# Performance work log

Hardware: AMD Instinct MI355X
Metric: run time of the kernel (lower is better)

Reference implementation:

```python
import jax, jax.numpy as jnp
import numpy as np

GRID = 480  # grid extent for both x and y voxel indices


def setup_inputs() -> dict:
    key = jax.random.key(0)
    k = jax.random.split(key, 8)
    B, N, FD, H1, H2, D = 4, 100000, 3, 128, 256, 64
    scale = 0.05
    pt_fea = jax.random.normal(k[0], (B, N, FD), dtype=jnp.float32)
    xy_ind = jax.random.randint(k[1], (B, N, 2), 0, GRID, dtype=jnp.int32)
    W1 = jax.random.normal(k[2], (FD, H1), dtype=jnp.float32) * scale
    b1 = jnp.zeros((H1,), dtype=jnp.float32)
    W2 = jax.random.normal(k[3], (H1, H2), dtype=jnp.float32) * scale
    b2 = jnp.zeros((H2,), dtype=jnp.float32)
    W3 = jax.random.normal(k[4], (H2, D), dtype=jnp.float32) * scale
    b3 = jnp.zeros((D,), dtype=jnp.float32)
    return {"pt_fea": pt_fea, "xy_ind": xy_ind, "W1": W1, "b1": b1,
            "W2": W2, "b2": b2, "W3": W3, "b3": b3}


def reference(pt_fea, xy_ind, W1, b1, W2, b2, W3, b3):
    B, N, FD = pt_fea.shape
    flat = pt_fea.reshape(B * N, FD)
    # pad xy_ind with batch id -> (b, x, y) per point
    bidx = jnp.repeat(jnp.arange(B, dtype=xy_ind.dtype), N)
    xy = xy_ind.reshape(B * N, 2)
    # lexicographic linear encoding so sorted linear order == torch.unique(dim=0) row order
    lin = (bidx.astype(jnp.int32) * GRID + xy[:, 0]) * GRID + xy[:, 1]
    unq_lin, unq_inv = jnp.unique(lin, return_inverse=True)
    M = int(unq_lin.shape[0])  # concrete: indices are concrete (eager unique)
    unq = jnp.stack([unq_lin // (GRID * GRID),
                     (unq_lin // GRID) % GRID,
                     unq_lin % GRID], axis=1)
    # per-point MLP: 3 -> 128 -> 256 -> 64
    h = jax.nn.relu(flat @ W1 + b1)
    h = jax.nn.relu(h @ W2 + b2)
    feat = h @ W3 + b3
    # scatter_max pooling per unique voxel
    pooled = jax.ops.segment_max(feat, unq_inv.reshape(-1), num_segments=M)
    return unq, pooled
```

## Files before the change

kernel.cpp:

```cpp
#include <hip/hip_runtime.h>
#include <hip/hip_bf16.h>

#define GRIDW 480
#define CELLS_PER_B (GRIDW*GRIDW)
#define NCELL (4*CELLS_PER_B)
#define NPTS  400000
#define NPB   100000
#define H1D 128
#define H2D 256
#define DD 64
#define SCAN_BLK 900
#define NTILE 6250
#define GRIDP 512
#define NSUB  25000
#define CNT_NB 1563

typedef unsigned short u16;
typedef __attribute__((ext_vector_type(8))) short bf16x8;
typedef __attribute__((ext_vector_type(4))) float f32x4;
typedef __attribute__((ext_vector_type(4))) unsigned u32x4;
typedef __attribute__((ext_vector_type(2))) unsigned u32x2;

static __device__ __forceinline__ u16 f2bf(float f){
  unsigned u = __float_as_uint(f);
  unsigned r = u + 0x7FFFu + ((u>>16)&1u);
  return (u16)(r>>16);
}
static __device__ __forceinline__ float bf2f(u16 b){
  return __uint_as_float(((unsigned)b) << 16);
}
static __device__ __forceinline__ unsigned cvt_pk_bf16(float lo, float hi){
  unsigned r;
  asm("v_cvt_pk_bf16_f32 %0, %1, %2" : "=v"(r) : "v"(lo), "v"(hi));
  return r;
}

static __device__ __forceinline__ void pack_one(int e, const float* W2, const float* W3,
                                                u16* bp2, u16* bp3){
  if (e < 32768){
    int j = e & 7, c = (e>>3)&15, ko = (e>>7)&15, n = e>>11;
    bp2[e] = f2bf(W2[(ko*8+j)*H2D + n*16 + c]);
  } else {
    int e3 = e - 32768;
    int j = e3 & 7, c = (e3>>3)&15, ko = (e3>>7)&31, n = e3>>12;
    bp3[e3] = f2bf(W3[(ko*8+j)*DD + n*16 + c]);
  }
}

__global__ void k_countpack(const int* __restrict__ xy, unsigned* __restrict__ counts,
                            const float* __restrict__ W2, const float* __restrict__ W3,
                            u16* __restrict__ bp2, u16* __restrict__ bp3){
  int b = blockIdx.x;
  if (b < CNT_NB){
    int p = b*256 + threadIdx.x;
    if (p < NPTS){
      int bb = p / NPB;
      int x = xy[2*p], y = xy[2*p+1];
      atomicAdd(&counts[(bb*GRIDW + x)*GRIDW + y], 1u);
    }
  } else {
    int e = (b - CNT_NB)*256 + threadIdx.x;
    if (e < 49152) pack_one(e, W2, W3, bp2, bp3);
  }
}

__global__ void k_scan2(const unsigned* __restrict__ counts,
                        unsigned* __restrict__ rankF, unsigned* __restrict__ rankC,
                        unsigned* __restrict__ bsumF, unsigned* __restrict__ bsumC){
  __shared__ unsigned shF[256], shC[256];
  int tid = threadIdx.x;
  int base = blockIdx.x*1024 + tid*4;
  unsigned c0=counts[base], c1=counts[base+1], c2=counts[base+2], c3=counts[base+3];
  unsigned f0=c0?1u:0u, f1=c1?1u:0u, f2=c2?1u:0u, f3=c3?1u:0u;
  unsigned sF=f0+f1+f2+f3, sC=c0+c1+c2+c3;
  shF[tid]=sF; shC[tid]=sC; __syncthreads();
  for (int off=1; off<256; off<<=1){
    unsigned tF = (tid>=off) ? shF[tid-off] : 0u;
    unsigned tC = (tid>=off) ? shC[tid-off] : 0u;
    __syncthreads();
    shF[tid] += tF; shC[tid] += tC;
    __syncthreads();
  }
  unsigned eF = shF[tid]-sF, eC = shC[tid]-sC;
  if (tid==255){ bsumF[blockIdx.x]=shF[255]; bsumC[blockIdx.x]=shC[255]; }
  rankF[base]=eF; rankF[base+1]=eF+f0; rankF[base+2]=eF+f0+f1; rankF[base+3]=eF+f0+f1+f2;
  rankC[base]=eC; rankC[base+1]=eC+c0; rankC[base+2]=eC+c0+c1; rankC[base+3]=eC+c0+c1+c2;
}

__global__ void k_scan_bsum2(unsigned* __restrict__ bsumF, unsigned* __restrict__ bsumC){
  __shared__ unsigned shF[1024], shC[1024];
  int tid = threadIdx.x;
  unsigned vF = (tid<SCAN_BLK) ? bsumF[tid] : 0u;
  unsigned vC = (tid<SCAN_BLK) ? bsumC[tid] : 0u;
  shF[tid]=vF; shC[tid]=vC; __syncthreads();
  for (int off=1; off<1024; off<<=1){
    unsigned tF = (tid>=off) ? shF[tid-off] : 0u;
    unsigned tC = (tid>=off) ? shC[tid-off] : 0u;
    __syncthreads();
    shF[tid] += tF; shC[tid] += tC;
    __syncthreads();
  }
  if (tid<SCAN_BLK){ bsumF[tid]=shF[tid]-vF; bsumC[tid]=shC[tid]-vC; }
}

__global__ void k_emit2(const unsigned* __restrict__ counts,
                        unsigned* __restrict__ rankF, unsigned* __restrict__ rankC,
                        const unsigned* __restrict__ bsumF, const unsigned* __restrict__ bsumC,
                        float* __restrict__ out){
  int i = blockIdx.x*256 + threadIdx.x;
  if (i >= NCELL) return;
  unsigned rF = rankF[i] + bsumF[i>>10];
  unsigned rC = rankC[i] + bsumC[i>>10];
  rankF[i] = rF; rankC[i] = rC;
  unsigned c = counts[i];
  if (c){
    int b = i / CELLS_PER_B;
    int rem = i - b*CELLS_PER_B;
    int x = rem / GRIDW;
    int y = rem - x*GRIDW;
    float* o = out + 3u*rF;
    o[0]=(float)b; o[1]=(float)x; o[2]=(float)y;
  }
}

__global__ void k_scatterp(const int* __restrict__ xy, unsigned* __restrict__ cursor,
                           const unsigned* __restrict__ rankF,
                           unsigned* __restrict__ perm, unsigned* __restrict__ vox){
  int p = blockIdx.x*256 + threadIdx.x;
  if (p >= NPTS) return;
  int b = p / NPB;
  int x = xy[2*p], y = xy[2*p+1];
  int cell = (b*GRIDW+x)*GRIDW + y;
  unsigned slot = atomicAdd(&cursor[cell], 1u);
  perm[slot] = (unsigned)p;
  vox[slot]  = rankF[cell];
}

__global__ __launch_bounds__(256,2) void k_mlpp(
    const float* __restrict__ pt, const unsigned* __restrict__ perm,
    const unsigned* __restrict__ vox,
    const u16* __restrict__ bp2, const u16* __restrict__ bp3,
    const float* __restrict__ W1, const float* __restrict__ b1,
    const float* __restrict__ b2, const float* __restrict__ b3,
    float* __restrict__ outp,
    unsigned* __restrict__ pvf, unsigned* __restrict__ pvl,
    u16* __restrict__ pmf, u16* __restrict__ pml)
{
  __shared__ __attribute__((aligned(16))) u16 h1s[64*128];
  __shared__ __attribute__((aligned(16))) u16 h2s[2][64*64];
  __shared__ __attribute__((aligned(16))) u16 w3s[16384];
  __shared__ __attribute__((aligned(16))) float cf[832];
  __shared__ __attribute__((aligned(16))) float in_s[192];
  __shared__ unsigned vox_s[64];

  const int tid  = threadIdx.x;
  const int lane = tid & 63;
  const int w    = tid >> 6;
  const int g    = lane >> 4;
  const int p    = lane & 15;
  const int wn   = w & 1;
  const int wp   = w >> 1;
  const int oct  = tid & 15;

  for (int i = tid; i < 2048; i += 256)
    *(u32x4*)((char*)w3s + i*16) = *(const u32x4*)((const char*)bp3 + i*16);
  for (int i = tid; i < 832; i += 256){
    float v;
    if (i < 384) v = W1[i];
    else if (i < 512) v = b1[i-384];
    else if (i < 768) v = b2[i-512];
    else v = b3[i-768];
    cf[i] = v;
  }

  bf16x8 wf2[32];
  #pragma unroll
  for (int c=0;c<4;++c)
    #pragma unroll
    for (int nn=0;nn<2;++nn)
      #pragma unroll
      for (int t=0;t<4;++t){
        int ngl = c*4 + 2*wn + nn;
        wf2[(c*2+nn)*4+t] = *(const bf16x8*)(bp2 + (((ngl*16 + t*4 + g)*16) + p)*8);
      }

  int tile = blockIdx.x;
  unsigned pmN = 0;
  float pf0=0.f, pf1=0.f, pf2=0.f;
  if (tid < 64){
    unsigned pm0 = perm[(size_t)tile*64 + tid];
    const float* q = pt + 3*(size_t)pm0;
    pf0 = q[0]; pf1 = q[1]; pf2 = q[2];
    if (tile + GRIDP < NTILE) pmN = perm[(size_t)(tile+GRIDP)*64 + tid];
  }
  __syncthreads();

  for (; tile < NTILE; tile += GRIDP){
    if (tid < 64){ in_s[tid*3]=pf0; in_s[tid*3+1]=pf1; in_s[tid*3+2]=pf2; }
    unsigned vr = 0;
    if (tid < 64) vr = vox[(size_t)tile*64 + tid];
    __syncthreads();
    if (tid < 64 && tile + GRIDP < NTILE){
      const float* q = pt + 3*(size_t)pmN;
      pf0 = q[0]; pf1 = q[1]; pf2 = q[2];
    }
    unsigned pmN2 = 0;
    if (tid < 64 && tile + 2*GRIDP < NTILE)
      pmN2 = perm[(size_t)(tile+2*GRIDP)*64 + tid];

    {
      f32x4 w1v[3][2], b1v[2];
      #pragma unroll
      for (int f=0;f<3;++f){
        w1v[f][0] = *(const f32x4*)&cf[f*128 + oct*8];
        w1v[f][1] = *(const f32x4*)&cf[f*128 + oct*8 + 4];
      }
      b1v[0] = *(const f32x4*)&cf[384 + oct*8];
      b1v[1] = *(const f32x4*)&cf[384 + oct*8 + 4];
      #pragma unroll
      for (int q=0;q<4;++q){
        int row = q*16 + (tid>>4);
        float x0 = in_s[row*3+0], x1 = in_s[row*3+1], x2 = in_s[row*3+2];
        f32x4 a0 = b1v[0], a1 = b1v[1];
        #pragma unroll
        for (int i=0;i<4;++i){
          a0[i] = fmaf(x0, w1v[0][0][i], a0[i]);
          a1[i] = fmaf(x0, w1v[0][1][i], a1[i]);
          a0[i] = fmaf(x1, w1v[1][0][i], a0[i]);
          a1[i] = fmaf(x1, w1v[1][1][i], a1[i]);
          a0[i] = fmaf(x2, w1v[2][0][i], a0[i]);
          a1[i] = fmaf(x2, w1v[2][1][i], a1[i]);
          a0[i] = fmaxf(a0[i], 0.f);
          a1[i] = fmaxf(a1[i], 0.f);
        }
        u32x4 ov;
        ov[0] = cvt_pk_bf16(a0[0], a0[1]);
        ov[1] = cvt_pk_bf16(a0[2], a0[3]);
        ov[2] = cvt_pk_bf16(a1[0], a1[1]);
        ov[3] = cvt_pk_bf16(a1[2], a1[3]);
        unsigned byte = ((unsigned)row<<8) + (unsigned)oct*16u;
        byte ^= (unsigned)(row&7) << 4;
        *(u32x4*)((char*)h1s + byte) = ov;
      }
    }
    if (tid < 64) vox_s[tid] = vr;
    __syncthreads();

    bf16x8 hf[2][4];
    #pragma unroll
    for (int pp=0;pp<2;++pp){
      int row = (2*wp+pp)*16 + p;
      #pragma unroll
      for (int t=0;t<4;++t){
        unsigned byte = ((unsigned)row<<8) + (unsigned)t*64u + (unsigned)g*16u;
        byte ^= (unsigned)(row&7) << 4;
        hf[pp][t] = *(const bf16x8*)((const char*)h1s + byte);
      }
    }

    f32x4 acc3[2][2];
    #pragma unroll
    for (int a=0;a<2;++a)
      #pragma unroll
      for (int b=0;b<2;++b){ acc3[a][b][0]=0.f; acc3[a][b][1]=0.f; acc3[a][b][2]=0.f; acc3[a][b][3]=0.f; }

    #pragma unroll
    for (int c=0;c<4;++c){
      f32x4 acc2[2][2];
      #pragma unroll
      for (int a=0;a<2;++a)
        #pragma unroll
        for (int b=0;b<2;++b){ acc2[a][b][0]=0.f; acc2[a][b][1]=0.f; acc2[a][b][2]=0.f; acc2[a][b][3]=0.f; }
      #pragma unroll
      for (int t=0;t<4;++t)
        #pragma unroll
        for (int nn=0;nn<2;++nn)
          #pragma unroll
          for (int pp=0;pp<2;++pp)
            acc2[nn][pp] = __builtin_amdgcn_mfma_f32_16x16x32_bf16(
                wf2[(c*2+nn)*4+t], hf[pp][t], acc2[nn][pp], 0, 0, 0);
      u16* h2 = h2s[c & 1];
      #pragma unroll
      for (int nn=0;nn<2;++nn){
        f32x4 b2v = *(const f32x4*)&cf[512 + c*64 + (2*wn+nn)*16 + g*4];
        #pragma unroll
        for (int pp=0;pp<2;++pp){
          int point = (2*wp+pp)*16 + p;
          float e0 = fmaxf(acc2[nn][pp][0] + b2v[0], 0.f);
          float e1 = fmaxf(acc2[nn][pp][1] + b2v[1], 0.f);
          float e2 = fmaxf(acc2[nn][pp][2] + b2v[2], 0.f);
          float e3 = fmaxf(acc2[nn][pp][3] + b2v[3], 0.f);
          u32x2 o2; o2[0] = cvt_pk_bf16(e0, e1); o2[1] = cvt_pk_bf16(e2, e3);
          unsigned byte = (unsigned)point*128u + (unsigned)((2*wn+nn)*32 + g*8);
          byte ^= (unsigned)(point&7) << 4;
          *(u32x2*)((char*)h2 + byte) = o2;
        }
      }
      __syncthreads();
      #pragma unroll
      for (int t2=0;t2<2;++t2){
        bf16x8 w3f[2], h2f[2];
        #pragma unroll
        for (int dn=0;dn<2;++dn){
          int dt = 2*wn + dn;
          unsigned wb = (unsigned)(((dt*32 + (c*2+t2)*4 + g)*16 + p)*16);
          w3f[dn] = *(const bf16x8*)((const char*)w3s + wb);
        }
        #pragma unroll
        for (int pp=0;pp<2;++pp){
          int point = (2*wp+pp)*16 + p;
          unsigned byte = (unsigned)point*128u + (unsigned)t2*64u + (unsigned)g*16u;
          byte ^= (unsigned)(point&7) << 4;
          h2f[pp] = *(const bf16x8*)((const char*)h2 + byte);
        }
        #pragma unroll
        for (int dn=0;dn<2;++dn)
          #pragma unroll
          for (int pp=0;pp<2;++pp)
            acc3[dn][pp] = __builtin_amdgcn_mfma_f32_16x16x32_bf16(
                w3f[dn], h2f[pp], acc3[dn][pp], 0, 0, 0);
      }
    }

    #pragma unroll
    for (int dn=0;dn<2;++dn){
      f32x4 b3v = *(const f32x4*)&cf[768 + (2*wn+dn)*16 + g*4];
      #pragma unroll
      for (int pp=0;pp<2;++pp){
        int point = (2*wp+pp)*16 + p;
        float e0 = acc3[dn][pp][0] + b3v[0];
        float e1 = acc3[dn][pp][1] + b3v[1];
        float e2 = acc3[dn][pp][2] + b3v[2];
        float e3 = acc3[dn][pp][3] + b3v[3];
        u32x2 o2; o2[0] = cvt_pk_bf16(e0, e1); o2[1] = cvt_pk_bf16(e2, e3);
        unsigned byte = (unsigned)point*128u + (unsigned)((2*wn+dn)*32 + g*8);
        byte ^= (unsigned)(point&7) << 4;
        *(u32x2*)((char*)h2s[0] + byte) = o2;
      }
    }
    __syncthreads();

    {
      int st = tile*4 + w;
      float val[16]; unsigned vid[16];
      #pragma unroll
      for (int r=0;r<16;++r){
        int row = w*16 + r;
        unsigned byte = (unsigned)row*128u + (unsigned)lane*2u;
        byte ^= (unsigned)(row&7) << 4;
        val[r] = bf2f(*(const u16*)((const char*)h2s[0] + byte));
        vid[r] = vox_s[row];
      }
      float m = val[0];
      unsigned vprev = vid[0];
      int runstart = 0;
      #pragma unroll
      for (int r=1;r<16;++r){
        if (vid[r] != vprev){
          if (runstart == 0){
            pmf[(size_t)st*64 + lane] = (u16)(__float_as_uint(m)>>16);
            if (lane==0) pvf[st] = vprev;
          } else {
            outp[(size_t)vprev*64 + lane] = m;
          }
          m = val[r]; runstart = r; vprev = vid[r];
        } else m = fmaxf(m, val[r]);
      }
      pml[(size_t)st*64 + lane] = (u16)(__float_as_uint(m)>>16);
      if (lane==0) pvl[st] = vprev;
      if (runstart == 0){
        pmf[(size_t)st*64 + lane] = (u16)(__float_as_uint(m)>>16);
        if (lane==0) pvf[st] = vprev;
      }
    }
    __syncthreads();
    pmN = pmN2;
  }
}

__global__ __launch_bounds__(256) void k_fixup(
    const unsigned* __restrict__ pvf, const unsigned* __restrict__ pvl,
    const u16* __restrict__ pmf, const u16* __restrict__ pml,
    float* __restrict__ outp){
  int t  = blockIdx.x*4 + (threadIdx.x>>6);
  int ch = threadIdx.x & 63;
  if (t >= NSUB) return;
  unsigned vf = pvf[t], vl = pvl[t];
  if (t == 0 || pvl[t-1] != vf){
    float m = bf2f(pmf[(size_t)t*64 + ch]);
    if (vl == vf){
      m = fmaxf(m, bf2f(pml[(size_t)t*64 + ch]));
      int k = t+1;
      while (k < NSUB && pvf[k] == vf){
        m = fmaxf(m, bf2f(pmf[(size_t)k*64 + ch]));
        if (pvl[k] != vf) break;
        m = fmaxf(m, bf2f(pml[(size_t)k*64 + ch]));
        ++k;
      }
    }
    outp[(size_t)vf*64 + ch] = m;
  }
  if (vl != vf){
    float m = bf2f(pml[(size_t)t*64 + ch]);
    int k = t+1;
    while (k < NSUB && pvf[k] == vl){
      m = fmaxf(m, bf2f(pmf[(size_t)k*64 + ch]));
      if (pvl[k] != vl) break;
      m = fmaxf(m, bf2f(pml[(size_t)k*64 + ch]));
      ++k;
    }
    outp[(size_t)vl*64 + ch] = m;
  }
}

extern "C" void kernel_launch(void* const* d_in, const int* in_sizes, int n_in,
                              void* d_out, int out_size, void* d_ws, size_t ws_size,
                              hipStream_t stream){
  const float* pt = (const float*)d_in[0];
  const int*   xy = (const int*)d_in[1];
  const float* W1 = (const float*)d_in[2];
  const float* b1 = (const float*)d_in[3];
  const float* W2 = (const float*)d_in[4];
  const float* b2 = (const float*)d_in[5];
  const float* W3 = (const float*)d_in[6];
  const float* b3 = (const float*)d_in[7];
  float* out = (float*)d_out;

  int M = out_size / 67;
  float* outp = out + 3*(size_t)M;

  unsigned* counts = (unsigned*)d_ws;
  unsigned* rankF  = counts + NCELL;
  unsigned* rankC  = rankF + NCELL;
  unsigned* bsumF  = rankC + NCELL;
  unsigned* bsumC  = bsumF + 1024;
  unsigned* perm   = bsumC + 1024;
  unsigned* vox    = perm + NPTS;
  unsigned* pvf    = vox + NPTS;
  unsigned* pvl    = pvf + NSUB;
  u16* bp2 = (u16*)(pvl + NSUB);
  u16* bp3 = bp2 + 32768;
  u16* pmf = bp3 + 16384;
  u16* pml = pmf + (size_t)NSUB*64;

  hipMemsetAsync(counts, 0, NCELL*sizeof(unsigned), stream);
  k_countpack  <<<CNT_NB+192, 256, 0, stream>>>(xy, counts, W2, W3, bp2, bp3);
  k_scan2      <<<SCAN_BLK, 256, 0, stream>>>(counts, rankF, rankC, bsumF, bsumC);
  k_scan_bsum2 <<<1, 1024, 0, stream>>>(bsumF, bsumC);
  k_emit2      <<<NCELL/256, 256, 0, stream>>>(counts, rankF, rankC, bsumF, bsumC, out);
  k_scatterp   <<<(NPTS+255)/256, 256, 0, stream>>>(xy, rankC, rankF, perm, vox);
  k_mlpp       <<<GRIDP, 256, 0, stream>>>(pt, perm, vox, bp2, bp3, W1, b1, b2, b3,
                                           outp, pvf, pvl, pmf, pml);
  k_fixup      <<<NSUB/4, 256, 0, stream>>>(pvf, pvl, pmf, pml, outp);
}
```

Measured before the change: 155.5 us.

## Fuse scan/emit/scatter kernels, drop W3 LDS staging, raise MLP occupancy

```diff
diff --git a/kernel.cpp b/kernel.cpp
--- a/kernel.cpp
+++ b/kernel.cpp
@@ -11,9 +11,10 @@
 #define DD 64
 #define SCAN_BLK 900
 #define NTILE 6250
-#define GRIDP 512
+#define GRIDP 768
 #define NSUB  25000
 #define CNT_NB 1563
+#define EMIT_NB 3600
 
 typedef unsigned short u16;
 typedef __attribute__((ext_vector_type(8))) short bf16x8;
@@ -66,8 +67,10 @@
 
 __global__ void k_scan2(const unsigned* __restrict__ counts,
                         unsigned* __restrict__ rankF, unsigned* __restrict__ rankC,
-                        unsigned* __restrict__ bsumF, unsigned* __restrict__ bsumC){
+                        unsigned* __restrict__ bsumF, unsigned* __restrict__ bsumC,
+                        unsigned* __restrict__ donecnt){
   __shared__ unsigned shF[256], shC[256];
+  __shared__ unsigned isLast;
   int tid = threadIdx.x;
   int base = blockIdx.x*1024 + tid*4;
   unsigned c0=counts[base], c1=counts[base+1], c2=counts[base+2], c3=counts[base+3];
@@ -85,58 +88,79 @@
   if (tid==255){ bsumF[blockIdx.x]=shF[255]; bsumC[blockIdx.x]=shC[255]; }
   rankF[base]=eF; rankF[base+1]=eF+f0; rankF[base+2]=eF+f0+f1; rankF[base+3]=eF+f0+f1+f2;
   rankC[base]=eC; rankC[base+1]=eC+c0; rankC[base+2]=eC+c0+c1; rankC[base+3]=eC+c0+c1+c2;
-}
-
-__global__ void k_scan_bsum2(unsigned* __restrict__ bsumF, unsigned* __restrict__ bsumC){
-  __shared__ unsigned shF[1024], shC[1024];
-  int tid = threadIdx.x;
-  unsigned vF = (tid<SCAN_BLK) ? bsumF[tid] : 0u;
-  unsigned vC = (tid<SCAN_BLK) ? bsumC[tid] : 0u;
-  shF[tid]=vF; shC[tid]=vC; __syncthreads();
-  for (int off=1; off<1024; off<<=1){
-    unsigned tF = (tid>=off) ? shF[tid-off] : 0u;
-    unsigned tC = (tid>=off) ? shC[tid-off] : 0u;
-    __syncthreads();
-    shF[tid] += tF; shC[tid] += tC;
-    __syncthreads();
-  }
-  if (tid<SCAN_BLK){ bsumF[tid]=shF[tid]-vF; bsumC[tid]=shC[tid]-vC; }
-}
-
-__global__ void k_emit2(const unsigned* __restrict__ counts,
-                        unsigned* __restrict__ rankF, unsigned* __restrict__ rankC,
-                        const unsigned* __restrict__ bsumF, const unsigned* __restrict__ bsumC,
-                        float* __restrict__ out){
-  int i = blockIdx.x*256 + threadIdx.x;
-  if (i >= NCELL) return;
-  unsigned rF = rankF[i] + bsumF[i>>10];
-  unsigned rC = rankC[i] + bsumC[i>>10];
-  rankF[i] = rF; rankC[i] = rC;
-  unsigned c = counts[i];
-  if (c){
-    int b = i / CELLS_PER_B;
-    int rem = i - b*CELLS_PER_B;
-    int x = rem / GRIDW;
-    int y = rem - x*GRIDW;
-    float* o = out + 3u*rF;
-    o[0]=(float)b; o[1]=(float)x; o[2]=(float)y;
-  }
-}
-
-__global__ void k_scatterp(const int* __restrict__ xy, unsigned* __restrict__ cursor,
-                           const unsigned* __restrict__ rankF,
-                           unsigned* __restrict__ perm, unsigned* __restrict__ vox){
-  int p = blockIdx.x*256 + threadIdx.x;
-  if (p >= NPTS) return;
-  int b = p / NPB;
-  int x = xy[2*p], y = xy[2*p+1];
-  int cell = (b*GRIDW+x)*GRIDW + y;
-  unsigned slot = atomicAdd(&cursor[cell], 1u);
-  perm[slot] = (unsigned)p;
-  vox[slot]  = rankF[cell];
-}
-
-__global__ __launch_bounds__(256,2) void k_mlpp(
+
+  __threadfence();
+  __syncthreads();
+  if (tid==0){
+    unsigned old = atomicAdd(donecnt, 1u);
+    isLast = (old == SCAN_BLK-1) ? 1u : 0u;
+  }
+  __syncthreads();
+  if (isLast){
+    __threadfence();
+    volatile unsigned* vF = (volatile unsigned*)bsumF;
+    volatile unsigned* vC = (volatile unsigned*)bsumC;
+    unsigned fv[4], cv[4];
+    int b4 = tid*4;
+    #pragma unroll
+    for (int j=0;j<4;++j){
+      fv[j] = (b4+j < SCAN_BLK) ? vF[b4+j] : 0u;
+      cv[j] = (b4+j < SCAN_BLK) ? vC[b4+j] : 0u;
+    }
+    unsigned tsF = fv[0]+fv[1]+fv[2]+fv[3], tsC = cv[0]+cv[1]+cv[2]+cv[3];
+    __syncthreads();
+    shF[tid]=tsF; shC[tid]=tsC; __syncthreads();
+    for (int off=1; off<256; off<<=1){
+      unsigned tF = (tid>=off) ? shF[tid-off] : 0u;
+      unsigned tC = (tid>=off) ? shC[tid-off] : 0u;
+      __syncthreads();
+      shF[tid] += tF; shC[tid] += tC;
+      __syncthreads();
+    }
+    unsigned pF = shF[tid]-tsF, pC = shC[tid]-tsC;
+    #pragma unroll
+    for (int j=0;j<4;++j){
+      if (b4+j < SCAN_BLK){
+        bsumF[b4+j] = pF; pF += fv[j];
+        bsumC[b4+j] = pC; pC += cv[j];
+      }
+    }
+  }
+}
+
+__global__ void k_emitscatter(
+    const unsigned* __restrict__ counts,
+    const unsigned* __restrict__ rankF, unsigned* __restrict__ rankC,
+    const unsigned* __restrict__ bsumF, const unsigned* __restrict__ bsumC,
+    const int* __restrict__ xy,
+    unsigned* __restrict__ perm, unsigned* __restrict__ vox,
+    float* __restrict__ out){
+  int b = blockIdx.x;
+  if (b < EMIT_NB){
+    int i = b*256 + threadIdx.x;
+    if (counts[i]){
+      unsigned rF = rankF[i] + bsumF[i>>10];
+      int bb = i / CELLS_PER_B;
+      int rem = i - bb*CELLS_PER_B;
+      int x = rem / GRIDW;
+      int y = rem - x*GRIDW;
+      float* o = out + 3u*rF;
+      o[0]=(float)bb; o[1]=(float)x; o[2]=(float)y;
+    }
+  } else {
+    int p = (b - EMIT_NB)*256 + threadIdx.x;
+    if (p < NPTS){
+      int bb = p / NPB;
+      int x = xy[2*p], y = xy[2*p+1];
+      int cell = (bb*GRIDW+x)*GRIDW + y;
+      unsigned slot = atomicAdd(&rankC[cell], 1u) + bsumC[cell>>10];
+      perm[slot] = (unsigned)p;
+      vox[slot]  = rankF[cell] + bsumF[cell>>10];
+    }
+  }
+}
+
+__global__ __launch_bounds__(256,3) void k_mlpp(
     const float* __restrict__ pt, const unsigned* __restrict__ perm,
     const unsigned* __restrict__ vox,
     const u16* __restrict__ bp2, const u16* __restrict__ bp3,
@@ -148,7 +172,6 @@
 {
   __shared__ __attribute__((aligned(16))) u16 h1s[64*128];
   __shared__ __attribute__((aligned(16))) u16 h2s[2][64*64];
-  __shared__ __attribute__((aligned(16))) u16 w3s[16384];
   __shared__ __attribute__((aligned(16))) float cf[832];
   __shared__ __attribute__((aligned(16))) float in_s[192];
   __shared__ unsigned vox_s[64];
@@ -162,8 +185,6 @@
   const int wp   = w >> 1;
   const int oct  = tid & 15;
 
-  for (int i = tid; i < 2048; i += 256)
-    *(u32x4*)((char*)w3s + i*16) = *(const u32x4*)((const char*)bp3 + i*16);
   for (int i = tid; i < 832; i += 256){
     float v;
     if (i < 384) v = W1[i];
@@ -185,28 +206,30 @@
       }
 
   int tile = blockIdx.x;
-  unsigned pmN = 0;
+  unsigned pmN = 0, vr = 0;
   float pf0=0.f, pf1=0.f, pf2=0.f;
-  if (tid < 64){
+  if (tid < 64 && tile < NTILE){
     unsigned pm0 = perm[(size_t)tile*64 + tid];
     const float* q = pt + 3*(size_t)pm0;
     pf0 = q[0]; pf1 = q[1]; pf2 = q[2];
+    vr = vox[(size_t)tile*64 + tid];
     if (tile + GRIDP < NTILE) pmN = perm[(size_t)(tile+GRIDP)*64 + tid];
   }
   __syncthreads();
 
   for (; tile < NTILE; tile += GRIDP){
-    if (tid < 64){ in_s[tid*3]=pf0; in_s[tid*3+1]=pf1; in_s[tid*3+2]=pf2; }
-    unsigned vr = 0;
-    if (tid < 64) vr = vox[(size_t)tile*64 + tid];
-    __syncthreads();
+    if (tid < 64){
+      in_s[tid*3]=pf0; in_s[tid*3+1]=pf1; in_s[tid*3+2]=pf2;
+      vox_s[tid]=vr;
+    }
+    __syncthreads();
+    float nf0=0.f, nf1=0.f, nf2=0.f; unsigned nvr=0, pmN2=0;
     if (tid < 64 && tile + GRIDP < NTILE){
       const float* q = pt + 3*(size_t)pmN;
-      pf0 = q[0]; pf1 = q[1]; pf2 = q[2];
-    }
-    unsigned pmN2 = 0;
-    if (tid < 64 && tile + 2*GRIDP < NTILE)
-      pmN2 = perm[(size_t)(tile+2*GRIDP)*64 + tid];
+      nf0 = q[0]; nf1 = q[1]; nf2 = q[2];
+      nvr = vox[(size_t)(tile+GRIDP)*64 + tid];
+      if (tile + 2*GRIDP < NTILE) pmN2 = perm[(size_t)(tile+2*GRIDP)*64 + tid];
+    }
 
     {
       f32x4 w1v[3][2], b1v[2];
@@ -243,7 +266,6 @@
         *(u32x4*)((char*)h1s + byte) = ov;
       }
     }
-    if (tid < 64) vox_s[tid] = vr;
     __syncthreads();
 
     bf16x8 hf[2][4];
@@ -303,8 +325,7 @@
         #pragma unroll
         for (int dn=0;dn<2;++dn){
           int dt = 2*wn + dn;
-          unsigned wb = (unsigned)(((dt*32 + (c*2+t2)*4 + g)*16 + p)*16);
-          w3f[dn] = *(const bf16x8*)((const char*)w3s + wb);
+          w3f[dn] = *(const bf16x8*)(bp3 + (((dt*32 + (c*2+t2)*4 + g)*16) + p)*8);
         }
         #pragma unroll
         for (int pp=0;pp<2;++pp){
@@ -374,7 +395,7 @@
       }
     }
     __syncthreads();
-    pmN = pmN2;
+    pf0=nf0; pf1=nf1; pf2=nf2; vr=nvr; pmN=pmN2;
   }
 }
 
@@ -429,26 +450,26 @@
   int M = out_size / 67;
   float* outp = out + 3*(size_t)M;
 
-  unsigned* counts = (unsigned*)d_ws;
-  unsigned* rankF  = counts + NCELL;
-  unsigned* rankC  = rankF + NCELL;
-  unsigned* bsumF  = rankC + NCELL;
-  unsigned* bsumC  = bsumF + 1024;
-  unsigned* perm   = bsumC + 1024;
-  unsigned* vox    = perm + NPTS;
-  unsigned* pvf    = vox + NPTS;
-  unsigned* pvl    = pvf + NSUB;
+  unsigned* counts  = (unsigned*)d_ws;
+  unsigned* donecnt = counts + NCELL;
+  unsigned* rankF   = donecnt + 1;
+  unsigned* rankC   = rankF + NCELL;
+  unsigned* bsumF   = rankC + NCELL;
+  unsigned* bsumC   = bsumF + 1024;
+  unsigned* perm    = bsumC + 1024;
+  unsigned* vox     = perm + NPTS;
+  unsigned* pvf     = vox + NPTS;
+  unsigned* pvl     = pvf + NSUB;
   u16* bp2 = (u16*)(pvl + NSUB);
   u16* bp3 = bp2 + 32768;
   u16* pmf = bp3 + 16384;
   u16* pml = pmf + (size_t)NSUB*64;
 
-  hipMemsetAsync(counts, 0, NCELL*sizeof(unsigned), stream);
+  hipMemsetAsync(counts, 0, (NCELL+1)*sizeof(unsigned), stream);
   k_countpack  <<<CNT_NB+192, 256, 0, stream>>>(xy, counts, W2, W3, bp2, bp3);
-  k_scan2      <<<SCAN_BLK, 256, 0, stream>>>(counts, rankF, rankC, bsumF, bsumC);
-  k_scan_bsum2 <<<1, 1024, 0, stream>>>(bsumF, bsumC);
-  k_emit2      <<<NCELL/256, 256, 0, stream>>>(counts, rankF, rankC, bsumF, bsumC, out);
-  k_scatterp   <<<(NPTS+255)/256, 256, 0, stream>>>(xy, rankC, rankF, perm, vox);
+  k_scan2      <<<SCAN_BLK, 256, 0, stream>>>(counts, rankF, rankC, bsumF, bsumC, donecnt);
+  k_emitscatter<<<EMIT_NB+CNT_NB, 256, 0, stream>>>(counts, rankF, rankC, bsumF, bsumC,
+                                                    xy, perm, vox, out);
   k_mlpp       <<<GRIDP, 256, 0, stream>>>(pt, perm, vox, bp2, bp3, W1, b1, b2, b3,
                                            outp, pvf, pvl, pmf, pml);
   k_fixup      <<<NSUB/4, 256, 0, stream>>>(pvf, pvl, pmf, pml, outp);
```

Result: slower. 379.6 us (+144.2%).
